# Kernel optimization log

Hardware: AMD Instinct MI355X
Metric: run time of the kernel (lower is better)

## Reference

```python
import jax, jax.numpy as jnp
import numpy as np
from jax import lax

DN = ('NHWC', 'HWIO', 'NHWC')

def conv2d_same(x, W, b):
    y = lax.conv_general_dilated(x, W, window_strides=(1, 1), padding='SAME', dimension_numbers=DN)
    return y + b

def maxpool2(x):
    # 2x2 max pool, stride 2, SAME padding (NHWC)
    return lax.reduce_window(x, -jnp.inf, lax.max, (1, 2, 2, 1), (1, 2, 2, 1), 'SAME')

def setup_inputs() -> dict:
    key = jax.random.key(0)
    ks = jax.random.split(key, 6)
    B, H, W, C = 8, 64, 64, 256
    s = 0.05
    return {
        'x': jax.random.normal(ks[0], (B, H, W, C), jnp.float32),
        'Wf': jax.random.normal(ks[1], (3, 3, C, C // 8), jnp.float32) * s,
        'bf': jnp.zeros((C // 8,), jnp.float32),
        'Wg': jax.random.normal(ks[2], (3, 3, C, C // 8), jnp.float32) * s,
        'bg': jnp.zeros((C // 8,), jnp.float32),
        'Wh': jax.random.normal(ks[3], (3, 3, C, C // 2), jnp.float32) * s,
        'bh': jnp.zeros((C // 2,), jnp.float32),
        'Wo': jax.random.normal(ks[4], (1, 1, C // 2, C), jnp.float32) * s,
        'bo': jnp.zeros((C,), jnp.float32),
        'gate': jnp.ones((1,), jnp.float32),
    }

def reference(x, Wf, bf, Wg, bg, Wh, bh, Wo, bo, gate):
    B, H, W, C = x.shape
    f = maxpool2(conv2d_same(x, Wf, bf))            # [B, H/2, W/2, C//8] keys
    g = conv2d_same(x, Wg, bg)                       # [B, H, W, C//8]     queries
    h = maxpool2(conv2d_same(x, Wh, bh))            # [B, H/2, W/2, C//2] values
    N, M = H * W, (H // 2) * (W // 2)
    gq = g.reshape(B, N, C // 8)
    fk = f.reshape(B, M, C // 8)
    hv = h.reshape(B, M, C // 2)
    attn = jax.nn.softmax(jnp.einsum('bnd,bmd->bnm', gq, fk), axis=-1)  # [B, N, M]
    wo = jnp.einsum('bnm,bmv->bnv', attn, hv).reshape(B, H, W, C // 2)
    out = conv2d_same(wo, Wo, bo)                    # [B, H, W, C]
    return x + gate[0] * out
```

## Files before the change

kernel.cpp:

```cpp
#include <hip/hip_runtime.h>
#include <hip/hip_fp16.h>

constexpr int B_  = 8;
constexpr int H_  = 64;
constexpr int W_  = 64;
constexpr int C_  = 256;
constexpr int CG_ = 32;
constexpr int CH_ = 128;
constexpr int NQ_ = 4096;
constexpr int NM_ = 1024;
constexpr int XP_ = 66;

constexpr int GP_ = 1048576;
constexpr int HP_ = 4194304;

typedef __attribute__((ext_vector_type(8))) _Float16 half8;
typedef __attribute__((ext_vector_type(4))) _Float16 half4;
typedef __attribute__((ext_vector_type(4))) float    f32x4;

__global__ void prep_xpad_k(const float* __restrict__ X, _Float16* __restrict__ Xpad) {
    int i8 = blockIdx.x * 256 + threadIdx.x;
    if (i8 >= B_ * XP_ * XP_ * 32) return;
    int c8 = i8 & 31;
    int px = i8 >> 5;
    int xx = px % XP_;
    int t  = px / XP_;
    int yy = t % XP_;
    int b  = t / XP_;
    half8 v;
    if (yy >= 1 && yy <= 64 && xx >= 1 && xx <= 64) {
        const float* s = X + (((size_t)(b * 64 + yy - 1) * 64) + (xx - 1)) * 256 + c8 * 8;
        float4 a = *reinterpret_cast<const float4*>(s);
        float4 bv = *reinterpret_cast<const float4*>(s + 4);
        v[0] = (_Float16)a.x;  v[1] = (_Float16)a.y;
        v[2] = (_Float16)a.z;  v[3] = (_Float16)a.w;
        v[4] = (_Float16)bv.x; v[5] = (_Float16)bv.y;
        v[6] = (_Float16)bv.z; v[7] = (_Float16)bv.w;
    } else {
        v = (half8)(_Float16)0.f;
    }
    *reinterpret_cast<half8*>(Xpad + (size_t)i8 * 8) = v;
}

__global__ void prep_wpk_k(const float* __restrict__ Wg, const float* __restrict__ Wf,
                           const float* __restrict__ Wh, _Float16* __restrict__ Wpk) {
    int i = blockIdx.x * 256 + threadIdx.x;
    if (i >= 12 * 9 * 8 * 64 * 8) return;
    int j    = i & 7;
    int lane = (i >> 3) & 63;
    int ks   = (i >> 9) & 7;
    int tap  = (i >> 12) % 9;
    int co16 = i / 36864;
    int lr = lane & 15, lk = lane >> 4;
    int co = co16 * 16 + lr;
    int kk = tap * 256 + ks * 32 + lk * 8 + j;
    float v;
    if (co < 32)      v = Wg[(size_t)kk * 32  + co];
    else if (co < 64) v = Wf[(size_t)kk * 32  + (co - 32)];
    else              v = Wh[(size_t)kk * 128 + (co - 64)];
    Wpk[i] = (_Float16)v;
}

__global__ void prep_bias_k(const float* __restrict__ bg, const float* __restrict__ bf,
                            const float* __restrict__ bh, float* __restrict__ bc) {
    int co = threadIdx.x;
    if (co >= 192) return;
    bc[co] = (co < 32) ? bg[co] : (co < 64) ? bf[co - 32] : bh[co - 64];
}

__global__ void prep_wok_k(const float* __restrict__ Wo, _Float16* __restrict__ Wok) {
    int i = blockIdx.x * 256 + threadIdx.x;
    if (i >= 16 * 4 * 64 * 8) return;
    int j    = i & 7;
    int lane = (i >> 3) & 63;
    int ks   = (i >> 9) & 3;
    int co16 = i >> 11;
    int co = co16 * 16 + (lane & 15);
    int k  = ks * 32 + (lane >> 4) * 8 + j;
    Wok[i] = (_Float16)Wo[(size_t)k * 256 + co];
}

__global__ __launch_bounds__(256, 4) void conv_mfma_k(
        const _Float16* __restrict__ Xpad, const _Float16* __restrict__ Wpk,
        const float* __restrict__ bc,
        _Float16* __restrict__ gpart, _Float16* __restrict__ fpart,
        _Float16* __restrict__ hpart) {
    __shared__ char lds[XP_ * 256 * 2];
    int bid = blockIdx.x;
    int lg  = (bid & 7) * 192 + (bid >> 3);
    int ky  = lg % 3;
    int iy  = lg / 3;
    int b   = iy >> 6;
    int y   = iy & 63;
    int tid = threadIdx.x;
    int wid = tid >> 6;
    int l   = tid & 63;
    int lr  = l & 15;
    int lk  = l >> 4;

    {
        const float4* sp = reinterpret_cast<const float4*>(
            Xpad + ((size_t)(b * XP_ + y + ky) * XP_) * 256);
        float4 vst[8];
#pragma unroll
        for (int j = 0; j < 8; ++j) vst[j] = sp[tid + j * 256];
        float4 tl;
        if (tid < 64) tl = sp[tid + 2048];
#pragma unroll
        for (int j = 0; j < 8; ++j) {
            int c = tid + j * 256; int px = c >> 5;
            *reinterpret_cast<float4*>(lds + ((c * 16) ^ ((px & 7) << 4))) = vst[j];
        }
        if (tid < 64) {
            int c = tid + 2048; int px = c >> 5;
            *reinterpret_cast<float4*>(lds + ((c * 16) ^ ((px & 7) << 4))) = tl;
        }
    }
    __syncthreads();

    f32x4 acc[4][3];
#pragma unroll
    for (int mi = 0; mi < 4; ++mi)
#pragma unroll
        for (int nj = 0; nj < 3; ++nj) acc[mi][nj] = (f32x4)0.f;

    auto ldw = [&](int tap, int ks, half8& d0, half8& d1, half8& d2) {
        const _Float16* p = Wpk + ((((size_t)(wid * 3) * 9 + tap) * 8 + ks) * 64 + l) * 8;
        d0 = *reinterpret_cast<const half8*>(p);
        d1 = *reinterpret_cast<const half8*>(p + 36864);
        d2 = *reinterpret_cast<const half8*>(p + 73728);
    };

    int tap0 = ky * 3;
    half8 b0, b1, b2, n0, n1, n2;
    ldw(tap0, 0, b0, b1, b2);
#pragma unroll
    for (int st = 0; st < 24; ++st) {
        int kx = st >> 3, ks = st & 7;
        if (st < 23) ldw(tap0 + ((st + 1) >> 3), (st + 1) & 7, n0, n1, n2);
        half8 af[4];
#pragma unroll
        for (int mi = 0; mi < 4; ++mi) {
            int px = mi * 16 + lr + kx;
            int ad = (px * 512 + ks * 64 + lk * 16) ^ ((px & 7) << 4);
            af[mi] = *reinterpret_cast<const half8*>(lds + ad);
        }
#pragma unroll
        for (int mi = 0; mi < 4; ++mi)
            acc[mi][0] = __builtin_amdgcn_mfma_f32_16x16x32_f16(af[mi], b0, acc[mi][0], 0, 0, 0);
#pragma unroll
        for (int mi = 0; mi < 4; ++mi)
            acc[mi][1] = __builtin_amdgcn_mfma_f32_16x16x32_f16(af[mi], b1, acc[mi][1], 0, 0, 0);
#pragma unroll
        for (int mi = 0; mi < 4; ++mi)
            acc[mi][2] = __builtin_amdgcn_mfma_f32_16x16x32_f16(af[mi], b2, acc[mi][2], 0, 0, 0);
        b0 = n0; b1 = n1; b2 = n2;
    }

    int pixbase = (b * 64 + y) * 64;
    bool addb = (ky == 1);
#pragma unroll
    for (int nj = 0; nj < 3; ++nj) {
        int co = wid * 48 + nj * 16 + lr;
        float bias = addb ? bc[co] : 0.f;
#pragma unroll
        for (int mi = 0; mi < 4; ++mi) {
#pragma unroll
            for (int r = 0; r < 4; ++r) {
                int x = mi * 16 + lk * 4 + r;
                float v = acc[mi][nj][r] + bias;
                size_t pix = pixbase + x;
                if (co < 32)
                    gpart[(size_t)ky * GP_ + pix * 32 + co] = (_Float16)(v * 1.44269504f);
                else if (co < 64)
                    fpart[(size_t)ky * GP_ + pix * 32 + (co - 32)] = (_Float16)v;
                else
                    hpart[(size_t)ky * HP_ + pix * 128 + (co - 64)] = (_Float16)v;
            }
        }
    }
}

__global__ void maxpool_f16_k(const _Float16* __restrict__ fp, _Float16* __restrict__ dst) {
    int i = blockIdx.x * 256 + threadIdx.x;
    if (i >= B_ * NM_ * CG_) return;
    int c = i & 31;
    int t = i >> 5;
    int px = t & 31;
    int py = (t >> 5) & 31;
    int b  = t >> 10;
    size_t base = (((size_t)(b * 64 + py * 2)) * 64 + px * 2) * 32 + c;
    const _Float16* p1 = fp + GP_;
    const _Float16* p2 = fp + 2 * GP_;
    auto val = [&](size_t o) { return (float)fp[o] + (float)p1[o] + (float)p2[o]; };
    float v = fmaxf(fmaxf(val(base), val(base + 32)),
                    fmaxf(val(base + 64 * 32), val(base + 64 * 32 + 32)));
    dst[i] = (_Float16)v;
}

__global__ __launch_bounds__(256) void vtpool_k(const _Float16* __restrict__ hp,
                                                _Float16* __restrict__ Vt) {
    __shared__ float t[32][33];
    int b  = blockIdx.x >> 7;
    int kt = (blockIdx.x >> 2) & 31;
    int ct = blockIdx.x & 3;
    int tid = threadIdx.x;
    const _Float16* p1 = hp + HP_;
    const _Float16* p2 = hp + 2 * (size_t)HP_;
#pragma unroll
    for (int i = 0; i < 4; ++i) {
        int e = tid + i * 256;
        int px = e >> 5, c = e & 31;
        size_t base = (((size_t)(b * 64 + kt * 2) * 64) + px * 2) * 128 + ct * 32 + c;
        auto val = [&](size_t o) { return (float)hp[o] + (float)p1[o] + (float)p2[o]; };
        float v = fmaxf(fmaxf(val(base), val(base + 128)),
                        fmaxf(val(base + 64 * 128), val(base + 64 * 128 + 128)));
        t[px][c] = v;
    }
    __syncthreads();
#pragma unroll
    for (int i = 0; i < 4; ++i) {
        int e = tid + i * 256;
        int c = e >> 5, px = e & 31;
        Vt[((size_t)b * 128 + ct * 32 + c) * 1024 + kt * 32 + px] = (_Float16)t[px][c];
    }
}

constexpr int PP_ = 72;

__global__ __launch_bounds__(256, 2) void attn_flash_k(
        const _Float16* __restrict__ Qp,
        const _Float16* __restrict__ Kf,
        const _Float16* __restrict__ Vt,
        _Float16* __restrict__ wo) {
    __shared__ _Float16 plds[4][16][PP_];
    __shared__ _Float16 vlds[2][8192];
    int bb  = blockIdx.x >> 6;
    int qt  = blockIdx.x & 63;
    int wid = threadIdx.x >> 6;
    int l   = threadIdx.x & 63;
    int lr  = l & 15;
    int lg  = l >> 4;
    int qbase = qt * 64 + wid * 16;

    const _Float16* gp = Qp + ((size_t)bb * NQ_ + qbase + lr) * 32 + lg * 8;
    half8 bq = *reinterpret_cast<const half8*>(gp);
    bq = bq + *reinterpret_cast<const half8*>(gp + GP_);
    bq = bq + *reinterpret_cast<const half8*>(gp + 2 * GP_);

    const _Float16* Kb = Kf + (size_t)bb * NM_ * 32;
    const _Float16* Vb = Vt + (size_t)bb * 128 * NM_;

    int o0  = wid * 4096 + l * 16;
    int vr0 = o0 >> 7;
    int vc  = (o0 >> 4) & 7;
    int vsw = (vr0 & 7) << 4;
    int lsw = (lr & 7) << 4;

    f32x4 acc[8];
#pragma unroll
    for (int vt = 0; vt < 8; ++vt) acc[vt] = (f32x4)0.f;
    float m_run = -1.0e30f;
    float l_lane = 0.f;

    half8 ak0, ak1, ak2, ak3;
    f32x4 s0, s1, s2, s3;
    half4 ph0, ph1, ph2, ph3;
    float4 vst[4];

#define STAGE_LOAD(T)                                                              \
    {   const _Float16* vp = Vb + (size_t)(T) * 64 + (size_t)vr0 * NM_ + vc * 8;   \
        vst[0] = *reinterpret_cast<const float4*>(vp);                             \
        vst[1] = *reinterpret_cast<const float4*>(vp + 8 * NM_);                   \
        vst[2] = *reinterpret_cast<const float4*>(vp + 16 * NM_);                  \
        vst[3] = *reinterpret_cast<const float4*>(vp + 24 * NM_);                  \
    }

#define STAGE_WRITE(BUF)                                                           \
    {   char* vbp = (char*)vlds[BUF] + (o0 ^ vsw);                                 \
        *reinterpret_cast<float4*>(vbp)        = vst[0];                           \
        *reinterpret_cast<float4*>(vbp + 1024) = vst[1];                           \
        *reinterpret_cast<float4*>(vbp + 2048) = vst[2];                           \
        *reinterpret_cast<float4*>(vbp + 3072) = vst[3];                           \
    }

#define LOADK(T)                                                                   \
    {   const _Float16* kp = Kb + (size_t)(T) * 64 * 32;                           \
        ak0 = *reinterpret_cast<const half8*>(kp + (size_t)(lr)      * 32 + lg*8); \
        ak1 = *reinterpret_cast<const half8*>(kp + (size_t)(16 + lr) * 32 + lg*8); \
        ak2 = *reinterpret_cast<const half8*>(kp + (size_t)(32 + lr) * 32 + lg*8); \
        ak3 = *reinterpret_cast<const half8*>(kp + (size_t)(48 + lr) * 32 + lg*8); \
    }

#define QK()                                                                \
    {   s0 = __builtin_amdgcn_mfma_f32_16x16x32_f16(ak0, bq, (f32x4)0.f, 0, 0, 0); \
        s1 = __builtin_amdgcn_mfma_f32_16x16x32_f16(ak1, bq, (f32x4)0.f, 0, 0, 0); \
        s2 = __builtin_amdgcn_mfma_f32_16x16x32_f16(ak2, bq, (f32x4)0.f, 0, 0, 0); \
        s3 = __builtin_amdgcn_mfma_f32_16x16x32_f16(ak3, bq, (f32x4)0.f, 0, 0, 0); \
    }

#define SOFTMAX()                                                           \
    {   float lm = fmaxf(fmaxf(fmaxf(s0[0], s0[1]), fmaxf(s0[2], s0[3])),   \
                         fmaxf(fmaxf(s1[0], s1[1]), fmaxf(s1[2], s1[3])));  \
        lm = fmaxf(lm, fmaxf(fmaxf(fmaxf(s2[0], s2[1]), fmaxf(s2[2], s2[3])), \
                             fmaxf(fmaxf(s3[0], s3[1]), fmaxf(s3[2], s3[3])))); \
        if (__any(lm > m_run + 11.0f)) {                                    \
            float mx = lm;                                                  \
            mx = fmaxf(mx, __shfl_xor(mx, 16, 64));                         \
            mx = fmaxf(mx, __shfl_xor(mx, 32, 64));                         \
            float mnew  = fmaxf(m_run, mx);                                 \
            float alpha = exp2f(m_run - mnew);                              \
            l_lane *= alpha;                                                \
            _Pragma("unroll")                                               \
            for (int r = 0; r < 4; ++r) {                                   \
                float ar = __shfl(alpha, 4 * lg + r, 64);                   \
                _Pragma("unroll")                                           \
                for (int vt = 0; vt < 8; ++vt) acc[vt][r] *= ar;            \
            }                                                               \
            m_run = mnew;                                                   \
        }                                                                   \
        float ps = 0.f;                                                     \
        {   float p0 = exp2f(s0[0]-m_run), p1 = exp2f(s0[1]-m_run);         \
            float p2 = exp2f(s0[2]-m_run), p3 = exp2f(s0[3]-m_run);         \
            ps += (p0+p1)+(p2+p3);                                          \
            ph0[0]=(_Float16)p0; ph0[1]=(_Float16)p1;                       \
            ph0[2]=(_Float16)p2; ph0[3]=(_Float16)p3; }                     \
        {   float p0 = exp2f(s1[0]-m_run), p1 = exp2f(s1[1]-m_run);         \
            float p2 = exp2f(s1[2]-m_run), p3 = exp2f(s1[3]-m_run);         \
            ps += (p0+p1)+(p2+p3);                                          \
            ph1[0]=(_Float16)p0; ph1[1]=(_Float16)p1;                       \
            ph1[2]=(_Float16)p2; ph1[3]=(_Float16)p3; }                     \
        {   float p0 = exp2f(s2[0]-m_run), p1 = exp2f(s2[1]-m_run);         \
            float p2 = exp2f(s2[2]-m_run), p3 = exp2f(s2[3]-m_run);         \
            ps += (p0+p1)+(p2+p3);                                          \
            ph2[0]=(_Float16)p0; ph2[1]=(_Float16)p1;                       \
            ph2[2]=(_Float16)p2; ph2[3]=(_Float16)p3; }                     \
        {   float p0 = exp2f(s3[0]-m_run), p1 = exp2f(s3[1]-m_run);         \
            float p2 = exp2f(s3[2]-m_run), p3 = exp2f(s3[3]-m_run);         \
            ps += (p0+p1)+(p2+p3);                                          \
            ph3[0]=(_Float16)p0; ph3[1]=(_Float16)p1;                       \
            ph3[2]=(_Float16)p2; ph3[3]=(_Float16)p3; }                     \
        l_lane += ps;                                                       \
    }

#define WRITEP()                                                            \
    {   *reinterpret_cast<half4*>(&plds[wid][lr][ 0 + 4*lg]) = ph0;         \
        *reinterpret_cast<half4*>(&plds[wid][lr][16 + 4*lg]) = ph1;         \
        *reinterpret_cast<half4*>(&plds[wid][lr][32 + 4*lg]) = ph2;         \
        *reinterpret_cast<half4*>(&plds[wid][lr][48 + 4*lg]) = ph3;         \
    }

#define PV(BUF)                                                             \
    {   half8 ap0 = *reinterpret_cast<const half8*>(&plds[wid][lr][8*lg]);  \
        half8 ap1 = *reinterpret_cast<const half8*>(&plds[wid][lr][32 + 8*lg]); \
        const char* vbp = (const char*)vlds[BUF];                           \
        _Pragma("unroll")                                                   \
        for (int vt = 0; vt < 8; ++vt) {                                    \
            int ra = (vt * 16 + lr) * 128;                                  \
            half8 bv = *reinterpret_cast<const half8*>(                     \
                vbp + ((ra + lg * 16) ^ lsw));                              \
            acc[vt] = __builtin_amdgcn_mfma_f32_16x16x32_f16(ap0, bv, acc[vt], 0, 0, 0); \
        }                                                                   \
        _Pragma("unroll")                                                   \
        for (int vt = 0; vt < 8; ++vt) {                                    \
            int ra = (vt * 16 + lr) * 128;                                  \
            half8 bv = *reinterpret_cast<const half8*>(                     \
                vbp + ((ra + (4 + lg) * 16) ^ lsw));                        \
            acc[vt] = __builtin_amdgcn_mfma_f32_16x16x32_f16(ap1, bv, acc[vt], 0, 0, 0); \
        }                                                                   \
    }

    STAGE_LOAD(0);
    STAGE_WRITE(0);
    LOADK(0);
    __syncthreads();
    QK(); SOFTMAX();

    for (int t = 0; t < 16; ++t) {
        if (t < 15) { STAGE_LOAD(t + 1); LOADK(t + 1); }
        WRITEP();
        PV(t & 1);
        if (t < 15) STAGE_WRITE((t + 1) & 1);
        __syncthreads();
        if (t < 15) { QK(); SOFTMAX(); }
    }

#undef STAGE_LOAD
#undef STAGE_WRITE
#undef LOADK
#undef QK
#undef SOFTMAX
#undef WRITEP
#undef PV

    float lsum = l_lane;
    lsum += __shfl_xor(lsum, 16, 64);
    lsum += __shfl_xor(lsum, 32, 64);
    float inv = 1.f / lsum;
#pragma unroll
    for (int r = 0; r < 4; ++r) {
        float ir = __shfl(inv, 4 * lg + r, 64);
        _Float16* orow = wo + ((size_t)bb * NQ_ + qbase + 4 * lg + r) * 128 + lr;
#pragma unroll
        for (int vt = 0; vt < 8; ++vt) orow[vt * 16] = (_Float16)(acc[vt][r] * ir);
    }
}

__global__ __launch_bounds__(256, 2) void conv1x1_mfma_k(
        const _Float16* __restrict__ wo, const _Float16* __restrict__ Wok,
        const float* __restrict__ bo, const float* __restrict__ X,
        const float* __restrict__ gate, float* __restrict__ out) {
    __shared__ char lds[64 * 256];
    int pix0 = blockIdx.x * 64;
    int tid = threadIdx.x;
    int wq = tid >> 6;
    int l  = tid & 63;
    int lr = l & 15;
    int lg = l >> 4;

    {
        const float4* sp = reinterpret_cast<const float4*>(wo + (size_t)pix0 * 128);
#pragma unroll
        for (int j = 0; j < 4; ++j) {
            int c = tid + j * 256;
            int px = c >> 4;
            *reinterpret_cast<float4*>(lds + ((c * 16) ^ ((px & 7) << 4))) = sp[c];
        }
    }
    __syncthreads();

    f32x4 acc[4][4];
#pragma unroll
    for (int mi = 0; mi < 4; ++mi)
#pragma unroll
        for (int nj = 0; nj < 4; ++nj) acc[mi][nj] = (f32x4)0.f;

#pragma unroll
    for (int ks = 0; ks < 4; ++ks) {
        half8 ap[4];
#pragma unroll
        for (int mi = 0; mi < 4; ++mi) {
            int px = mi * 16 + lr;
            int ad = (px * 256 + ks * 64 + lg * 16) ^ ((px & 7) << 4);
            ap[mi] = *reinterpret_cast<const half8*>(lds + ad);
        }
#pragma unroll
        for (int nj = 0; nj < 4; ++nj) {
            int co16 = wq * 4 + nj;
            half8 bv = *reinterpret_cast<const half8*>(
                Wok + (((size_t)co16 * 4 + ks) * 64 + l) * 8);
#pragma unroll
            for (int mi = 0; mi < 4; ++mi)
                acc[mi][nj] = __builtin_amdgcn_mfma_f32_16x16x32_f16(ap[mi], bv, acc[mi][nj], 0, 0, 0);
        }
    }

    float gt = gate[0];
#pragma unroll
    for (int nj = 0; nj < 4; ++nj) {
        int co = wq * 64 + nj * 16 + lr;
        float bias = bo[co];
#pragma unroll
        for (int mi = 0; mi < 4; ++mi) {
#pragma unroll
            for (int r = 0; r < 4; ++r) {
                size_t o = (size_t)(pix0 + mi * 16 + lg * 4 + r) * 256 + co;
                out[o] = X[o] + gt * (acc[mi][nj][r] + bias);
            }
        }
    }
}

extern "C" void kernel_launch(void* const* d_in, const int* in_sizes, int n_in,
                              void* d_out, int out_size, void* d_ws, size_t ws_size,
                              hipStream_t stream) {
    const float* X    = (const float*)d_in[0];
    const float* Wf   = (const float*)d_in[1];
    const float* bf   = (const float*)d_in[2];
    const float* Wg   = (const float*)d_in[3];
    const float* bg   = (const float*)d_in[4];
    const float* Wh   = (const float*)d_in[5];
    const float* bh   = (const float*)d_in[6];
    const float* Wo   = (const float*)d_in[7];
    const float* bo   = (const float*)d_in[8];
    const float* gate = (const float*)d_in[9];
    float* out = (float*)d_out;

    _Float16* gpart = (_Float16*)d_ws;
    _Float16* fpart = gpart + 3 * (size_t)GP_;
    _Float16* hpart = fpart + 3 * (size_t)GP_;
    _Float16* Kf    = hpart + 3 * (size_t)HP_;
    _Float16* Vt    = Kf + 262144;
    _Float16* Xpad  = Vt + 1048576;
    _Float16* Wpk   = Xpad + 8921088;
    float*    bc    = (float*)(Wpk + 442368);
    _Float16* Wok   = (_Float16*)(bc + 192);
    _Float16* wobuf = hpart;

    prep_xpad_k<<<(B_ * XP_ * XP_ * 32 + 255) / 256, 256, 0, stream>>>(X, Xpad);
    prep_wpk_k<<<(12 * 9 * 8 * 64 * 8 + 255) / 256, 256, 0, stream>>>(Wg, Wf, Wh, Wpk);
    prep_bias_k<<<1, 256, 0, stream>>>(bg, bf, bh, bc);
    prep_wok_k<<<(16 * 4 * 64 * 8 + 255) / 256, 256, 0, stream>>>(Wo, Wok);
    conv_mfma_k<<<3 * B_ * H_, 256, 0, stream>>>(Xpad, Wpk, bc, gpart, fpart, hpart);
    maxpool_f16_k<<<(B_ * NM_ * CG_ + 255) / 256, 256, 0, stream>>>(fpart, Kf);
    vtpool_k<<<B_ * 32 * 4, 256, 0, stream>>>(hpart, Vt);
    attn_flash_k<<<B_ * 64, 256, 0, stream>>>(gpart, Kf, Vt, wobuf);
    conv1x1_mfma_k<<<(B_ * NQ_) / 64, 256, 0, stream>>>(wobuf, Wok, bo, X, gate, out);
}
```

Baseline: 113.6 us.

## Fuse input padding/fp16 conversion into conv kernel and merge weight prep kernels

Removes the separate Xpad pre-pass: the conv kernel now reads fp32 X directly, converts to fp16 and zero-pads on the fly while filling LDS. The three weight/bias prep kernels are merged into one launch, and the weight prefetch in the conv main loop goes from one stage ahead to two using a 3-slot register ring. This drops a full fp16 write and re-read of the padded input plus three launches, but each conv block now reads fp32 input (twice the bytes per row, three times across ky) and uses more registers for the deeper prefetch.

```diff
diff --git a/kernel.cpp b/kernel.cpp
--- a/kernel.cpp
+++ b/kernel.cpp
@@ -18,70 +18,46 @@
 typedef __attribute__((ext_vector_type(4))) _Float16 half4;
 typedef __attribute__((ext_vector_type(4))) float    f32x4;
 
-__global__ void prep_xpad_k(const float* __restrict__ X, _Float16* __restrict__ Xpad) {
-    int i8 = blockIdx.x * 256 + threadIdx.x;
-    if (i8 >= B_ * XP_ * XP_ * 32) return;
-    int c8 = i8 & 31;
-    int px = i8 >> 5;
-    int xx = px % XP_;
-    int t  = px / XP_;
-    int yy = t % XP_;
-    int b  = t / XP_;
-    half8 v;
-    if (yy >= 1 && yy <= 64 && xx >= 1 && xx <= 64) {
-        const float* s = X + (((size_t)(b * 64 + yy - 1) * 64) + (xx - 1)) * 256 + c8 * 8;
-        float4 a = *reinterpret_cast<const float4*>(s);
-        float4 bv = *reinterpret_cast<const float4*>(s + 4);
-        v[0] = (_Float16)a.x;  v[1] = (_Float16)a.y;
-        v[2] = (_Float16)a.z;  v[3] = (_Float16)a.w;
-        v[4] = (_Float16)bv.x; v[5] = (_Float16)bv.y;
-        v[6] = (_Float16)bv.z; v[7] = (_Float16)bv.w;
-    } else {
-        v = (half8)(_Float16)0.f;
-    }
-    *reinterpret_cast<half8*>(Xpad + (size_t)i8 * 8) = v;
-}
-
-__global__ void prep_wpk_k(const float* __restrict__ Wg, const float* __restrict__ Wf,
-                           const float* __restrict__ Wh, _Float16* __restrict__ Wpk) {
+__global__ void prep_w_k(const float* __restrict__ Wg, const float* __restrict__ Wf,
+                         const float* __restrict__ Wh, const float* __restrict__ Wo,
+                         const float* __restrict__ bg, const float* __restrict__ bf,
+                         const float* __restrict__ bh,
+                         _Float16* __restrict__ Wpk, _Float16* __restrict__ Wok,
+                         float* __restrict__ bc) {
     int i = blockIdx.x * 256 + threadIdx.x;
-    if (i >= 12 * 9 * 8 * 64 * 8) return;
-    int j    = i & 7;
-    int lane = (i >> 3) & 63;
-    int ks   = (i >> 9) & 7;
-    int tap  = (i >> 12) % 9;
-    int co16 = i / 36864;
-    int lr = lane & 15, lk = lane >> 4;
-    int co = co16 * 16 + lr;
-    int kk = tap * 256 + ks * 32 + lk * 8 + j;
-    float v;
-    if (co < 32)      v = Wg[(size_t)kk * 32  + co];
-    else if (co < 64) v = Wf[(size_t)kk * 32  + (co - 32)];
-    else              v = Wh[(size_t)kk * 128 + (co - 64)];
-    Wpk[i] = (_Float16)v;
-}
-
-__global__ void prep_bias_k(const float* __restrict__ bg, const float* __restrict__ bf,
-                            const float* __restrict__ bh, float* __restrict__ bc) {
-    int co = threadIdx.x;
-    if (co >= 192) return;
-    bc[co] = (co < 32) ? bg[co] : (co < 64) ? bf[co - 32] : bh[co - 64];
-}
-
-__global__ void prep_wok_k(const float* __restrict__ Wo, _Float16* __restrict__ Wok) {
-    int i = blockIdx.x * 256 + threadIdx.x;
-    if (i >= 16 * 4 * 64 * 8) return;
-    int j    = i & 7;
-    int lane = (i >> 3) & 63;
-    int ks   = (i >> 9) & 3;
-    int co16 = i >> 11;
-    int co = co16 * 16 + (lane & 15);
-    int k  = ks * 32 + (lane >> 4) * 8 + j;
-    Wok[i] = (_Float16)Wo[(size_t)k * 256 + co];
+    if (i < 12 * 9 * 8 * 64 * 8) {
+        int j    = i & 7;
+        int lane = (i >> 3) & 63;
+        int ks   = (i >> 9) & 7;
+        int tap  = (i >> 12) % 9;
+        int co16 = i / 36864;
+        int co = co16 * 16 + (lane & 15);
+        int kk = tap * 256 + ks * 32 + (lane >> 4) * 8 + j;
+        float v;
+        if (co < 32)      v = Wg[(size_t)kk * 32  + co];
+        else if (co < 64) v = Wf[(size_t)kk * 32  + (co - 32)];
+        else              v = Wh[(size_t)kk * 128 + (co - 64)];
+        Wpk[i] = (_Float16)v;
+        return;
+    }
+    int i2 = i - 12 * 9 * 8 * 64 * 8;
+    if (i2 < 16 * 4 * 64 * 8) {
+        int j    = i2 & 7;
+        int lane = (i2 >> 3) & 63;
+        int ks   = (i2 >> 9) & 3;
+        int co16 = i2 >> 11;
+        int co = co16 * 16 + (lane & 15);
+        int k  = ks * 32 + (lane >> 4) * 8 + j;
+        Wok[i2] = (_Float16)Wo[(size_t)k * 256 + co];
+        return;
+    }
+    int co = i2 - 16 * 4 * 64 * 8;
+    if (co < 192)
+        bc[co] = (co < 32) ? bg[co] : (co < 64) ? bf[co - 32] : bh[co - 64];
 }
 
 __global__ __launch_bounds__(256, 4) void conv_mfma_k(
-        const _Float16* __restrict__ Xpad, const _Float16* __restrict__ Wpk,
+        const float* __restrict__ X, const _Float16* __restrict__ Wpk,
         const float* __restrict__ bc,
         _Float16* __restrict__ gpart, _Float16* __restrict__ fpart,
         _Float16* __restrict__ hpart) {
@@ -92,6 +68,7 @@
     int iy  = lg / 3;
     int b   = iy >> 6;
     int y   = iy & 63;
+    int yy  = y + ky - 1;
     int tid = threadIdx.x;
     int wid = tid >> 6;
     int l   = tid & 63;
@@ -99,21 +76,35 @@
     int lk  = l >> 4;
 
     {
-        const float4* sp = reinterpret_cast<const float4*>(
-            Xpad + ((size_t)(b * XP_ + y + ky) * XP_) * 256);
-        float4 vst[8];
-#pragma unroll
-        for (int j = 0; j < 8; ++j) vst[j] = sp[tid + j * 256];
-        float4 tl;
-        if (tid < 64) tl = sp[tid + 2048];
-#pragma unroll
-        for (int j = 0; j < 8; ++j) {
-            int c = tid + j * 256; int px = c >> 5;
-            *reinterpret_cast<float4*>(lds + ((c * 16) ^ ((px & 7) << 4))) = vst[j];
-        }
-        if (tid < 64) {
-            int c = tid + 2048; int px = c >> 5;
-            *reinterpret_cast<float4*>(lds + ((c * 16) ^ ((px & 7) << 4))) = tl;
+        bool rowok = (yy >= 0 && yy < 64);
+        const float* xrow = X + ((size_t)(b * 64 + yy) * 64) * 256;
+        half8 vst[9];
+#pragma unroll
+        for (int j = 0; j < 9; ++j) {
+            int c = tid + j * 256;
+            half8 v = (half8)(_Float16)0.f;
+            if (j < 8 || tid < 64) {
+                int px = c >> 5;
+                int ch = (c & 31) * 8;
+                if (rowok && px >= 1 && px <= 64) {
+                    const float* s = xrow + (size_t)(px - 1) * 256 + ch;
+                    float4 a  = *reinterpret_cast<const float4*>(s);
+                    float4 b2 = *reinterpret_cast<const float4*>(s + 4);
+                    v[0] = (_Float16)a.x;  v[1] = (_Float16)a.y;
+                    v[2] = (_Float16)a.z;  v[3] = (_Float16)a.w;
+                    v[4] = (_Float16)b2.x; v[5] = (_Float16)b2.y;
+                    v[6] = (_Float16)b2.z; v[7] = (_Float16)b2.w;
+                }
+            }
+            vst[j] = v;
+        }
+#pragma unroll
+        for (int j = 0; j < 9; ++j) {
+            int c = tid + j * 256;
+            if (j < 8 || tid < 64) {
+                int px = c >> 5;
+                *reinterpret_cast<half8*>(lds + ((c * 16) ^ ((px & 7) << 4))) = vst[j];
+            }
         }
     }
     __syncthreads();
@@ -124,20 +115,22 @@
 #pragma unroll
         for (int nj = 0; nj < 3; ++nj) acc[mi][nj] = (f32x4)0.f;
 
-    auto ldw = [&](int tap, int ks, half8& d0, half8& d1, half8& d2) {
-        const _Float16* p = Wpk + ((((size_t)(wid * 3) * 9 + tap) * 8 + ks) * 64 + l) * 8;
-        d0 = *reinterpret_cast<const half8*>(p);
-        d1 = *reinterpret_cast<const half8*>(p + 36864);
-        d2 = *reinterpret_cast<const half8*>(p + 73728);
+    int tap0 = ky * 3;
+    auto ldw = [&](int s, half8* d) {
+        const _Float16* p = Wpk +
+            ((((size_t)(wid * 3) * 9 + tap0 + (s >> 3)) * 8 + (s & 7)) * 64 + l) * 8;
+        d[0] = *reinterpret_cast<const half8*>(p);
+        d[1] = *reinterpret_cast<const half8*>(p + 36864);
+        d[2] = *reinterpret_cast<const half8*>(p + 73728);
     };
 
-    int tap0 = ky * 3;
-    half8 b0, b1, b2, n0, n1, n2;
-    ldw(tap0, 0, b0, b1, b2);
+    half8 wb[3][3];
+    ldw(0, wb[0]);
+    ldw(1, wb[1]);
 #pragma unroll
     for (int st = 0; st < 24; ++st) {
+        if (st < 22) ldw(st + 2, wb[(st + 2) % 3]);
         int kx = st >> 3, ks = st & 7;
-        if (st < 23) ldw(tap0 + ((st + 1) >> 3), (st + 1) & 7, n0, n1, n2);
         half8 af[4];
 #pragma unroll
         for (int mi = 0; mi < 4; ++mi) {
@@ -145,16 +138,16 @@
             int ad = (px * 512 + ks * 64 + lk * 16) ^ ((px & 7) << 4);
             af[mi] = *reinterpret_cast<const half8*>(lds + ad);
         }
+        const half8* w = wb[st % 3];
 #pragma unroll
         for (int mi = 0; mi < 4; ++mi)
-            acc[mi][0] = __builtin_amdgcn_mfma_f32_16x16x32_f16(af[mi], b0, acc[mi][0], 0, 0, 0);
+            acc[mi][0] = __builtin_amdgcn_mfma_f32_16x16x32_f16(af[mi], w[0], acc[mi][0], 0, 0, 0);
 #pragma unroll
         for (int mi = 0; mi < 4; ++mi)
-            acc[mi][1] = __builtin_amdgcn_mfma_f32_16x16x32_f16(af[mi], b1, acc[mi][1], 0, 0, 0);
+            acc[mi][1] = __builtin_amdgcn_mfma_f32_16x16x32_f16(af[mi], w[1], acc[mi][1], 0, 0, 0);
 #pragma unroll
         for (int mi = 0; mi < 4; ++mi)
-            acc[mi][2] = __builtin_amdgcn_mfma_f32_16x16x32_f16(af[mi], b2, acc[mi][2], 0, 0, 0);
-        b0 = n0; b1 = n1; b2 = n2;
+            acc[mi][2] = __builtin_amdgcn_mfma_f32_16x16x32_f16(af[mi], w[2], acc[mi][2], 0, 0, 0);
     }
 
     int pixbase = (b * 64 + y) * 64;
@@ -491,17 +484,14 @@
     _Float16* hpart = fpart + 3 * (size_t)GP_;
     _Float16* Kf    = hpart + 3 * (size_t)HP_;
     _Float16* Vt    = Kf + 262144;
-    _Float16* Xpad  = Vt + 1048576;
-    _Float16* Wpk   = Xpad + 8921088;
+    _Float16* Wpk   = Vt + 1048576;
     float*    bc    = (float*)(Wpk + 442368);
     _Float16* Wok   = (_Float16*)(bc + 192);
     _Float16* wobuf = hpart;
 
-    prep_xpad_k<<<(B_ * XP_ * XP_ * 32 + 255) / 256, 256, 0, stream>>>(X, Xpad);
-    prep_wpk_k<<<(12 * 9 * 8 * 64 * 8 + 255) / 256, 256, 0, stream>>>(Wg, Wf, Wh, Wpk);
-    prep_bias_k<<<1, 256, 0, stream>>>(bg, bf, bh, bc);
-    prep_wok_k<<<(16 * 4 * 64 * 8 + 255) / 256, 256, 0, stream>>>(Wo, Wok);
-    conv_mfma_k<<<3 * B_ * H_, 256, 0, stream>>>(Xpad, Wpk, bc, gpart, fpart, hpart);
+    prep_w_k<<<(12*9*8*64*8 + 16*4*64*8 + 192 + 255) / 256, 256, 0, stream>>>(
+        Wg, Wf, Wh, Wo, bg, bf, bh, Wpk, Wok, bc);
+    conv_mfma_k<<<3 * B_ * H_, 256, 0, stream>>>(X, Wpk, bc, gpart, fpart, hpart);
     maxpool_f16_k<<<(B_ * NM_ * CG_ + 255) / 256, 256, 0, stream>>>(fpart, Kf);
     vtpool_k<<<B_ * 32 * 4, 256, 0, stream>>>(hpart, Vt);
     attn_flash_k<<<B_ * 64, 256, 0, stream>>>(gpart, Kf, Vt, wobuf);
```

Result: faster. 107.9 us (-5.0%).
